# Kernel tuning notes

Measured on AMD Instinct MI355X. Metric: run time of the kernel, lower is better.

Reference implementation:

```python
import jax, jax.numpy as jnp
import numpy as np

N_QUBITS = 7
DEPTH = 2
DIM = 2 ** N_QUBITS  # 128
BATCH = 262144

# Qiskit little-endian convention: statevector index bit q = (idx >> q) & 1.
_idx = np.arange(DIM)
_bits = (_idx[:, None] >> np.arange(N_QUBITS)) & 1            # (DIM, N_QUBITS)
# CZ on all adjacent pairs (q, q+1): sign = (-1)^sum(bit_q * bit_{q+1})
_cz_parity = np.sum(_bits[:, :-1] * _bits[:, 1:], axis=1) % 2
CZ_PHASE = jnp.asarray(1.0 - 2.0 * _cz_parity, dtype=jnp.float32)   # (DIM,)
# Z_i expectation signs: <Z_i> = sum_idx p(idx) * (1 - 2*bit_i)
Z_SIGNS = jnp.asarray(1.0 - 2.0 * _bits, dtype=jnp.float32)         # (DIM, N_QUBITS)


def _apply_ry(state, q, theta_q):
    # state: (B, DIM) real amplitudes; RY is real so state stays real.
    lo = 2 ** q
    hi = DIM // (2 * lo)
    s = state.reshape(-1, hi, 2, lo)
    half = theta_q * 0.5
    c, sn = jnp.cos(half), jnp.sin(half)
    a0, a1 = s[:, :, 0, :], s[:, :, 1, :]
    out = jnp.stack([c * a0 - sn * a1, sn * a0 + c * a1], axis=2)
    return out.reshape(-1, DIM)


def setup_inputs() -> dict:
    key = jax.random.key(0)
    k1, k2 = jax.random.split(key)
    embed = jax.random.normal(k1, (BATCH, DIM), dtype=jnp.float32)
    theta = jax.random.normal(k2, (DEPTH * N_QUBITS,), dtype=jnp.float32) * 0.1
    return {"embed": embed, "theta": theta}


def reference(embed, theta):
    # Amplitude encoding: L2-normalize each row.
    state = embed / jnp.linalg.norm(embed, axis=1, keepdims=True)
    for d in range(DEPTH):
        for q in range(N_QUBITS):
            state = _apply_ry(state, q, theta[d * N_QUBITS + q])
        state = state * CZ_PHASE[None, :]
    probs = state * state                  # (B, DIM)
    return probs @ Z_SIGNS                 # (B, N_QUBITS)
```

## Files before the change

kernel.cpp:

```cpp
#include <hip/hip_runtime.h>
#include <utility>

#define NQ   7
#define DIM  128
#define HALF 64
#define RPB  32

template<class F, int... I>
__device__ __forceinline__ void static_for_impl(F&& f, std::integer_sequence<int, I...>) {
    (f(std::integral_constant<int, I>{}), ...);
}
template<int N, class F>
__device__ __forceinline__ void static_for(F&& f) {
    static_for_impl(static_cast<F&&>(f), std::make_integer_sequence<int, N>{});
}

__device__ __forceinline__ float swap_adj(float x) {
    int v = __builtin_amdgcn_update_dpp(0, __builtin_bit_cast(int, x),
                                        0xB1 ,
                                        0xF, 0xF, true);
    return __builtin_bit_cast(float, v);
}

__global__ __launch_bounds__(64, 2)
void qnat_kernel(const float* __restrict__ embed,
                 const float* __restrict__ theta,
                 float* __restrict__ out)
{
    __shared__ float4 tile[RPB * 33];
    const int lane = threadIdx.x;
    const int t = lane >> 1;
    const int h = lane & 1;
    const float4* __restrict__ g4 =
        reinterpret_cast<const float4*>(embed) + (size_t)blockIdx.x * (RPB * 32);

    static_for<16>([&](auto J) {
        constexpr int j = J.value;
        const float4 v = g4[j * 64 + lane];
        tile[(2 * j + (lane >> 5)) * 33 + (lane & 31)] = v;
    });
    __syncthreads();

    float st[HALF];
    static_for<16>([&](auto J) {
        constexpr int j = J.value;
        const float4 v = tile[t * 33 + h * 16 + j];
        st[4 * j + 0] = v.x;
        st[4 * j + 1] = v.y;
        st[4 * j + 2] = v.z;
        st[4 * j + 3] = v.w;
    });

    float ss = 0.f;
    static_for<HALF>([&](auto I) {
        constexpr int i = I.value;
        ss = fmaf(st[i], st[i], ss);
    });
    ss += swap_adj(ss);

    const float hs = h ? -1.f : 1.f;

    static_for<2>([&](auto D) {
        constexpr int d = D.value;
        static_for<6>([&](auto Q) {
            constexpr int q = Q.value;
            const float ha = 0.5f * theta[d * NQ + q];
            const float c_ = __cosf(ha), s_ = __sinf(ha);
            static_for<32>([&](auto P) {
                constexpr int p  = P.value;
                constexpr int lo = 1 << q;
                constexpr int i0 = ((p >> q) << (q + 1)) | (p & (lo - 1));
                constexpr int i1 = i0 | lo;
                const float a0 = st[i0], a1 = st[i1];
                st[i0] = fmaf(c_, a0, -s_ * a1);
                st[i1] = fmaf(s_, a0,  c_ * a1);
            });
        });
        {
            const float ha = 0.5f * theta[d * NQ + 6];
            const float c_ = __cosf(ha), s_ = __sinf(ha);
            const float sgn = h ? s_ : -s_;
            static_for<HALF>([&](auto J) {
                constexpr int j = J.value;
                const float other = swap_adj(st[j]);
                st[j] = fmaf(sgn, other, c_ * st[j]);
            });
        }
        static_for<HALF>([&](auto J) {
            constexpr int j = J.value;
            if constexpr ((__builtin_popcount(j & (j >> 1)) & 1) == 1) st[j] = -st[j];
            if constexpr (((j >> 5) & 1) == 1) st[j] *= hs;
        });
    });

    static_for<HALF>([&](auto J) {
        constexpr int j = J.value;
        st[j] *= st[j];
    });

    float o[NQ];
    static_for<6>([&](auto K) {
        constexpr int k = K.value;
        constexpr int n = HALF >> (k + 1);
        float acc = 0.f;
        static_for<32>([&](auto I) {
            constexpr int i = I.value;
            if constexpr (i < n) {
                const float a = st[2 * i], b = st[2 * i + 1];
                acc += a - b;
                st[i] = a + b;
            }
        });
        o[k] = acc;
    });
    static_for<6>([&](auto K) {
        constexpr int k = K.value;
        o[k] += swap_adj(o[k]);
    });
    {
        const float part = st[0];
        o[6] = hs * (part - swap_adj(part));
    }
    const float invss = __builtin_amdgcn_rcpf(ss);
    static_for<NQ>([&](auto K) { o[K.value] *= invss; });

    __syncthreads();
    float* ldsf = reinterpret_cast<float*>(tile);
    if (h == 0) {
        static_for<NQ>([&](auto K) {
            constexpr int k = K.value;
            ldsf[t * NQ + k] = o[k];
        });
    }
    __syncthreads();
    float* __restrict__ ob = out + (size_t)blockIdx.x * (RPB * NQ);
    static_for<4>([&](auto It) {
        constexpr int it = It.value;
        const int idx = it * 64 + lane;
        if constexpr (it < 3) {
            ob[idx] = ldsf[idx];
        } else {
            if (idx < RPB * NQ) ob[idx] = ldsf[idx];
        }
    });
}

extern "C" void kernel_launch(void* const* d_in, const int* in_sizes, int n_in,
                              void* d_out, int out_size, void* d_ws, size_t ws_size,
                              hipStream_t stream)
{
    const float* embed = (const float*)d_in[0];
    const float* theta = (const float*)d_in[1];
    float* out = (float*)d_out;
    const int batch = in_sizes[0] / DIM;
    dim3 grid(batch / RPB), block(64);
    hipLaunchKernelGGL(qnat_kernel, grid, block, 0, stream, embed, theta, out);
}
```

Before: 193.0 us.

## Issue all global loads up front, halve LDS tile, fold CZ phases into rotations

Issues all 16 float4 global loads into registers before any LDS traffic, then stages the rows through a half-size LDS tile in two rounds, so global latency overlaps and LDS use drops. The CZ sign flips are folded into the next layer's RY coefficients and operand negations, removing a separate elementwise pass. The final CZ of depth 1 is dropped because it does not change squared amplitudes. The norm sum is split into four accumulators to break the dependency chain. In exchange the kernel holds more live registers and adds extra barriers.

```diff
diff --git a/kernel.cpp b/kernel.cpp
--- a/kernel.cpp
+++ b/kernel.cpp
@@ -27,38 +27,65 @@
                  const float* __restrict__ theta,
                  float* __restrict__ out)
 {
-    __shared__ float4 tile[RPB * 33];
+    __shared__ float4 tile[16 * 33];
     const int lane = threadIdx.x;
     const int t = lane >> 1;
     const int h = lane & 1;
+    const float hs = h ? -1.f : 1.f;
     const float4* __restrict__ g4 =
         reinterpret_cast<const float4*>(embed) + (size_t)blockIdx.x * (RPB * 32);
 
-    static_for<16>([&](auto J) {
+    float4 A[8], B[8];
+    static_for<8>([&](auto J) {
         constexpr int j = J.value;
-        const float4 v = g4[j * 64 + lane];
-        tile[(2 * j + (lane >> 5)) * 33 + (lane & 31)] = v;
+        A[j] = g4[j * 64 + lane];
+    });
+    static_for<8>([&](auto J) {
+        constexpr int j = J.value;
+        B[j] = g4[512 + j * 64 + lane];
+    });
+
+    float st[HALF];
+
+    static_for<8>([&](auto J) {
+        constexpr int j = J.value;
+        tile[(2 * j + (lane >> 5)) * 33 + (lane & 31)] = A[j];
     });
     __syncthreads();
+    if (t < 16) {
+        static_for<16>([&](auto J) {
+            constexpr int j = J.value;
+            const float4 v = tile[t * 33 + h * 16 + j];
+            st[4 * j + 0] = v.x; st[4 * j + 1] = v.y;
+            st[4 * j + 2] = v.z; st[4 * j + 3] = v.w;
+        });
+    }
+    __syncthreads();
 
-    float st[HALF];
-    static_for<16>([&](auto J) {
+    static_for<8>([&](auto J) {
         constexpr int j = J.value;
-        const float4 v = tile[t * 33 + h * 16 + j];
-        st[4 * j + 0] = v.x;
-        st[4 * j + 1] = v.y;
-        st[4 * j + 2] = v.z;
-        st[4 * j + 3] = v.w;
+        tile[(2 * j + (lane >> 5)) * 33 + (lane & 31)] = B[j];
     });
+    __syncthreads();
+    if (t >= 16) {
+        static_for<16>([&](auto J) {
+            constexpr int j = J.value;
+            const float4 v = tile[(t - 16) * 33 + h * 16 + j];
+            st[4 * j + 0] = v.x; st[4 * j + 1] = v.y;
+            st[4 * j + 2] = v.z; st[4 * j + 3] = v.w;
+        });
+    }
 
-    float ss = 0.f;
-    static_for<HALF>([&](auto I) {
+    float s0 = 0.f, s1 = 0.f, s2 = 0.f, s3 = 0.f;
+    static_for<16>([&](auto I) {
         constexpr int i = I.value;
-        ss = fmaf(st[i], st[i], ss);
+        s0 = fmaf(st[4 * i + 0], st[4 * i + 0], s0);
+        s1 = fmaf(st[4 * i + 1], st[4 * i + 1], s1);
+        s2 = fmaf(st[4 * i + 2], st[4 * i + 2], s2);
+        s3 = fmaf(st[4 * i + 3], st[4 * i + 3], s3);
     });
+    float ss = (s0 + s1) + (s2 + s3);
     ss += swap_adj(ss);
-
-    const float hs = h ? -1.f : 1.f;
 
     static_for<2>([&](auto D) {
         constexpr int d = D.value;
@@ -66,14 +93,21 @@
             constexpr int q = Q.value;
             const float ha = 0.5f * theta[d * NQ + q];
             const float c_ = __cosf(ha), s_ = __sinf(ha);
+            const float sA = (d == 1 && q == 5) ? s_ * hs : s_;
+            const float cA = (d == 1 && q == 5) ? c_ * hs : c_;
             static_for<32>([&](auto P) {
                 constexpr int p  = P.value;
                 constexpr int lo = 1 << q;
                 constexpr int i0 = ((p >> q) << (q + 1)) | (p & (lo - 1));
                 constexpr int i1 = i0 | lo;
-                const float a0 = st[i0], a1 = st[i1];
-                st[i0] = fmaf(c_, a0, -s_ * a1);
-                st[i1] = fmaf(s_, a0,  c_ * a1);
+                constexpr bool n0 = (d == 1 && q == 0) &&
+                                    (__builtin_popcount(i0 & (i0 >> 1)) & 1);
+                constexpr bool n1 = (d == 1 && q == 0) &&
+                                    (__builtin_popcount(i1 & (i1 >> 1)) & 1);
+                const float a0 = n0 ? -st[i0] : st[i0];
+                const float a1 = n1 ? -st[i1] : st[i1];
+                st[i0] = fmaf(c_, a0, -sA * a1);
+                st[i1] = fmaf(s_, a0,  cA * a1);
             });
         });
         {
@@ -86,11 +120,6 @@
                 st[j] = fmaf(sgn, other, c_ * st[j]);
             });
         }
-        static_for<HALF>([&](auto J) {
-            constexpr int j = J.value;
-            if constexpr ((__builtin_popcount(j & (j >> 1)) & 1) == 1) st[j] = -st[j];
-            if constexpr (((j >> 5) & 1) == 1) st[j] *= hs;
-        });
     });
 
     static_for<HALF>([&](auto J) {
```

New measurement: 212.9 us. 1.1x slower.
